# Kernel tuning notes

Measured on AMD Instinct MI355X. Metric: run time of the kernel, lower is better.

## Reference

```python
import jax, jax.numpy as jnp
import numpy as np

HPC = 42  # HPC_FEATURES_LEN

def setup_inputs() -> dict:
    key = jax.random.key(0)
    ks = jax.random.split(key, 8)
    B, N, C, P, S = 4, 16384, 103, 2048, 32
    xyz = jax.random.normal(ks[0], (B, N, 3), dtype=jnp.float32)
    features = jax.random.normal(ks[1], (B, C, N), dtype=jnp.float32)
    new_xyz = jax.random.normal(ks[2], (B, P, 3), dtype=jnp.float32)
    idx = jax.random.randint(ks[3], (B, P, S), 0, N, dtype=jnp.int32)
    # 1x1-conv weights (out_ch, in_ch); gate conv sees full 3+C=106 channels
    Wg = jax.random.normal(ks[4], (64, 106), dtype=jnp.float32) * 0.05
    bg = jnp.zeros((64,), dtype=jnp.float32)
    W1 = jax.random.normal(ks[5], (64, 64), dtype=jnp.float32) * 0.05
    b1 = jnp.zeros((64,), dtype=jnp.float32)
    W2 = jax.random.normal(ks[6], (128, 64), dtype=jnp.float32) * 0.05
    b2 = jnp.zeros((128,), dtype=jnp.float32)
    W3 = jax.random.normal(ks[7], (256, 128), dtype=jnp.float32) * 0.05
    b3 = jnp.zeros((256,), dtype=jnp.float32)
    return {"xyz": xyz, "features": features, "new_xyz": new_xyz, "idx": idx,
            "Wg": Wg, "bg": bg, "W1": W1, "b1": b1, "W2": W2, "b2": b2,
            "W3": W3, "b3": b3}

def reference(xyz, features, new_xyz, idx, Wg, bg, W1, b1, W2, b2, W3, b3):
    # --- grouping: gather neighbors, center xyz, concat features ---
    # grouped_xyz: (B, P, S, 3) -> (B, 3, P, S)
    grouped_xyz = jax.vmap(lambda x, i: x[i])(xyz, idx) - new_xyz[:, :, None, :]
    grouped_xyz = jnp.transpose(grouped_xyz, (0, 3, 1, 2))
    # grouped_feat: (B, C, P, S)
    grouped_feat = jax.vmap(lambda f, i: f[:, i])(features, idx)
    nf = jnp.concatenate([grouped_xyz, grouped_feat], axis=1)  # (B, 3+C, P, S)
    base = nf[:, :-HPC]                                        # (B, 3+C-42, P, S)
    # --- gating 1x1 conv on full channels, then elementwise gate ---
    w = jnp.einsum('bcps,oc->bops', nf, Wg) + bg[None, :, None, None]
    x = base * (1.0 + w)
    # --- 1x1-conv MLP stack with ReLU ---
    for W, b in ((W1, b1), (W2, b2), (W3, b3)):
        x = jax.nn.relu(jnp.einsum('bcps,oc->bops', x, W) + b[None, :, None, None])
    # --- max pool over nsample ---
    pooled = jnp.max(x, axis=-1)  # (B, 256, P)
    return new_xyz, pooled
```

## Files before the change

### kernel.cpp

```cpp
#include <hip/hip_runtime.h>
#include <stdint.h>


namespace {
constexpr int kB = 4, kN = 16384, kC = 103, kP = 2048, kS = 32;

using short8 = __attribute__((ext_vector_type(8))) short;
using short4 = __attribute__((ext_vector_type(4))) short;
using f32x4  = __attribute__((ext_vector_type(4))) float;

constexpr int WG_HI = 0,     WG_LO = 8192;
constexpr int W1_HI = 16384, W1_LO = 20480;
constexpr int W2_HI = 24576, W2_LO = 32768;
constexpr int W3_HI = 40960, W3_LO = 73728;
constexpr size_t FT_OFF    = 262144;
constexpr size_t FT_SHORTS = (size_t)kB * kN * 128;
constexpr size_t WS_NEED   = FT_OFF + 2 * FT_SHORTS * 2;

__device__ __forceinline__ unsigned short f2bf(float x) {
    unsigned u = __float_as_uint(x);
    u += 0x7fffu + ((u >> 16) & 1u);
    return (unsigned short)(u >> 16);
}
__device__ __forceinline__ float bf2f(unsigned short h) {
    return __uint_as_float((unsigned)h << 16);
}
__device__ __forceinline__ unsigned cvtpk(float a, float b) {
    unsigned r;
    asm("v_cvt_pk_bf16_f32 %0, %1, %2" : "=v"(r) : "v"(a), "v"(b));
    return r;
}
__device__ __forceinline__ void pack4(const float v[4], uint2& H, uint2& L) {
    H.x = cvtpk(v[0], v[1]);
    H.y = cvtpk(v[2], v[3]);
    const float r0 = v[0] - __uint_as_float(H.x << 16);
    const float r1 = v[1] - __uint_as_float(H.x & 0xffff0000u);
    const float r2 = v[2] - __uint_as_float(H.y << 16);
    const float r3 = v[3] - __uint_as_float(H.y & 0xffff0000u);
    L.x = cvtpk(r0, r1);
    L.y = cvtpk(r2, r3);
}

__global__ void copy_newxyz(const float* __restrict__ src, float* __restrict__ dst, int n) {
    int i = blockIdx.x * blockDim.x + threadIdx.x;
    if (i < n) dst[i] = src[i];
}

__global__ void prep_weights(const float* __restrict__ Wg, const float* __restrict__ W1,
                             const float* __restrict__ W2, const float* __restrict__ W3,
                             short* __restrict__ ws) {
    int i = blockIdx.x * blockDim.x + threadIdx.x;
    if (i >= 53248) return;
    float w; int hi, lo, j;
    if (i < 8192)       { j = i;         int o = j >> 7, c = j & 127; w = (c < 106) ? Wg[o * 106 + c] : 0.f; hi = WG_HI; lo = WG_LO; }
    else if (i < 12288) { j = i - 8192;  int o = j >> 6, c = j & 63;  w = W1[o * 64 + c];  hi = W1_HI; lo = W1_LO; }
    else if (i < 20480) { j = i - 12288; int o = j >> 6, c = j & 63;  w = W2[o * 64 + c];  hi = W2_HI; lo = W2_LO; }
    else                { j = i - 20480; int o = j >> 7, c = j & 127; w = W3[o * 128 + c]; hi = W3_HI; lo = W3_LO; }
    unsigned short h = f2bf(w);
    ws[hi + j] = (short)h;
    ws[lo + j] = (short)f2bf(w - bf2f(h));
}

__global__ __launch_bounds__(512) void prep_feat(const float* __restrict__ f,
                                                 short* __restrict__ ftH, short* __restrict__ ftL) {
    __shared__ float tile[kC][65];
    const int bb = blockIdx.x >> 8;
    const int n0 = (blockIdx.x & 255) * 64;
    const int tid = threadIdx.x;
    for (int c = tid >> 6; c < kC; c += 8)
        tile[c][tid & 63] = f[((size_t)bb * kC + c) * kN + n0 + (tid & 63)];
    __syncthreads();
    const int np = tid >> 3, gc = tid & 7;
    short* rH = ftH + ((size_t)bb * kN + n0 + np) * 128;
    short* rL = ftL + ((size_t)bb * kN + n0 + np) * 128;
    #pragma unroll
    for (int kk = 0; kk < 2; ++kk) {
        const int chunk = gc + 8 * kk;
        union { uint4 u; short s[8]; } H, L;
        #pragma unroll
        for (int e = 0; e < 8; ++e) {
            const int col = chunk * 8 + e;
            float v = (col >= 3 && col < 106) ? tile[col - 3][np] : 0.f;
            unsigned short hh = f2bf(v);
            H.s[e] = (short)hh;
            L.s[e] = (short)f2bf(v - bf2f(hh));
        }
        *(uint4*)(rH + chunk * 8) = H.u;
        *(uint4*)(rL + chunk * 8) = L.u;
    }
}

template<int NOT, int NPT, int KT, int LDC, int LDW, bool INIT>
__device__ __forceinline__ void gemm_core(
    const short* __restrict__ xh, const short* __restrict__ xl,
    const short* __restrict__ wh, const short* __restrict__ wl,
    const float* __restrict__ bias, int kwoff,
    int ot0, int pt0t, int lane, f32x4 (&acc)[NOT][NPT])
{
    const int q = lane >> 4, n16 = lane & 15;
    short8 whr[NOT * KT], wlr[NOT * KT];
    #pragma unroll
    for (int i = 0; i < NOT; ++i)
        #pragma unroll
        for (int kt = 0; kt < KT; ++kt) {
            const size_t we = (size_t)((ot0 + i) * 16 + n16) * LDW + kwoff + kt * 32 + q * 8;
            whr[i * KT + kt] = *(const short8*)(wh + we);
            wlr[i * KT + kt] = *(const short8*)(wl + we);
        }
    if constexpr (INIT) {
        #pragma unroll
        for (int i = 0; i < NOT; ++i) {
            const f32x4 binit = *(const f32x4*)(bias + (ot0 + i) * 16 + 4 * q);
            #pragma unroll
            for (int j = 0; j < NPT; ++j) acc[i][j] = binit;
        }
    }
    #pragma unroll
    for (int kt = 0; kt < KT; ++kt) {
        const int k0 = kt * 32 + q * 8;
        short8 bh[NPT], bl[NPT];
        #pragma unroll
        for (int j = 0; j < NPT; ++j) {
            const int p = (pt0t + j) * 16 + n16;
            const int e = p * LDC + (k0 ^ ((p & 7) << 3));
            bh[j] = *(const short8*)(xh + e);
            bl[j] = *(const short8*)(xl + e);
        }
        #pragma unroll
        for (int i = 0; i < NOT; ++i) {
            const short8 ah = whr[i * KT + kt];
            const short8 al = wlr[i * KT + kt];
            #pragma unroll
            for (int j = 0; j < NPT; ++j) {
                acc[i][j] = __builtin_amdgcn_mfma_f32_16x16x32_bf16(ah, bh[j], acc[i][j], 0, 0, 0);
                acc[i][j] = __builtin_amdgcn_mfma_f32_16x16x32_bf16(ah, bl[j], acc[i][j], 0, 0, 0);
                acc[i][j] = __builtin_amdgcn_mfma_f32_16x16x32_bf16(al, bh[j], acc[i][j], 0, 0, 0);
            }
        }
    }
}

template<int NOT, int NPT, bool GATE, int LDCO>
__device__ __forceinline__ void store_act(
    f32x4 (&acc)[NOT][NPT], short* __restrict__ oh, short* __restrict__ ol,
    const short* __restrict__ nfh, const short* __restrict__ nfl,
    int ot0, int pt0t, int lane)
{
    const int q = lane >> 4, n16 = lane & 15;
    #pragma unroll
    for (int i = 0; i < NOT; ++i) {
        const int ob = (ot0 + i) * 16 + 4 * q;
        #pragma unroll
        for (int j = 0; j < NPT; ++j) {
            const int p = (pt0t + j) * 16 + n16;
            const int cs = ob ^ ((p & 7) << 3);
            float v[4];
            if (GATE) {
                const short4 h4 = *(const short4*)(nfh + p * 128 + cs);
                const short4 l4 = *(const short4*)(nfl + p * 128 + cs);
                #pragma unroll
                for (int r = 0; r < 4; ++r) {
                    const float base = bf2f((unsigned short)h4[r]) + bf2f((unsigned short)l4[r]);
                    v[r] = fmaf(base, acc[i][j][r], base);
                }
            } else {
                #pragma unroll
                for (int r = 0; r < 4; ++r) v[r] = fmaxf(acc[i][j][r], 0.f);
            }
            uint2 H, L;
            pack4(v, H, L);
            *(uint2*)(oh + p * LDCO + cs) = H;
            *(uint2*)(ol + p * LDCO + cs) = L;
        }
    }
}

template<bool DENSE>
__global__ __launch_bounds__(512, 2) void pointnet_sa(
    const float* __restrict__ xyz, const float* __restrict__ features,
    const float* __restrict__ new_xyz, const int* __restrict__ idx,
    const short* __restrict__ ws, const short* __restrict__ ftH, const short* __restrict__ ftL,
    const float* __restrict__ bg, const float* __restrict__ b1,
    const float* __restrict__ b2, const float* __restrict__ b3,
    float* __restrict__ out_pooled)
{
    __shared__ alignas(16) short smem[24576];
    short* NFh = smem;
    short* NFl = smem + 8192;
    short* X0h = smem + 16384;
    short* X0l = smem + 20480;

    const int tid = threadIdx.x, lane = tid & 63, wave = tid >> 6;
    const int q = lane >> 4, n16 = lane & 15;
    const int pt0 = blockIdx.x * 64;
    const int b = pt0 >> 16;

    if (DENSE) {
        const int gp = tid >> 3, gc = tid & 7;
        const int pt = pt0 + gp;
        const int n = idx[pt];
        const short* rH = ftH + ((size_t)b * kN + n) * 128;
        const short* rL = ftL + ((size_t)b * kN + n) * 128;
        uint4 hc0 = *(const uint4*)(rH + gc * 8);
        uint4 hc1 = *(const uint4*)(rH + gc * 8 + 64);
        uint4 lc0 = *(const uint4*)(rL + gc * 8);
        uint4 lc1 = *(const uint4*)(rL + gc * 8 + 64);
        if (gc == 0) {
            const float* xp = xyz + ((size_t)b * kN + n) * 3;
            const int pp = (pt >> 5) & (kP - 1);
            const float* np = new_xyz + ((size_t)b * kP + pp) * 3;
            union { uint4 u; short s[8]; } H, L;
            H.u = hc0; L.u = lc0;
            #pragma unroll
            for (int c = 0; c < 3; ++c) {
                const float v = xp[c] - np[c];
                const unsigned short hh = f2bf(v);
                H.s[c] = (short)hh;
                L.s[c] = (short)f2bf(v - bf2f(hh));
            }
            hc0 = H.u; lc0 = L.u;
        }
        const int sw = (gc ^ (gp & 7)) * 8;
        *(uint4*)(NFh + gp * 128 + sw)      = hc0;
        *(uint4*)(NFh + gp * 128 + sw + 64) = hc1;
        *(uint4*)(NFl + gp * 128 + sw)      = lc0;
        *(uint4*)(NFl + gp * 128 + sw + 64) = lc1;
    } else {
        const int p = tid & 63;
        const int cg = tid >> 6;
        const int pt = pt0 + p;
        const int n = idx[pt];
        const int pp = (pt >> 5) & (kP - 1);
        const float* fbp = features + (size_t)b * kC * kN + n;
        const float* xp = xyz + ((size_t)b * kN + n) * 3;
        const float* np = new_xyz + ((size_t)b * kP + pp) * 3;
        for (int c = cg; c < 128; c += 8) {
            float v;
            if (c < 3)        v = xp[c] - np[c];
            else if (c < 106) v = fbp[(size_t)(c - 3) * kN];
            else              v = 0.f;
            const unsigned short h = f2bf(v);
            const int cs = c ^ ((p & 7) << 3);
            NFh[p * 128 + cs] = (short)h;
            NFl[p * 128 + cs] = (short)f2bf(v - bf2f(h));
        }
    }
    __syncthreads();

    {
        f32x4 a[1][2];
        gemm_core<1, 2, 4, 128, 128, true>(NFh, NFl, ws + WG_HI, ws + WG_LO, bg, 0,
                                           wave & 3, 2 * (wave >> 2), lane, a);
        store_act<1, 2, true, 64>(a, X0h, X0l, NFh, NFl, wave & 3, 2 * (wave >> 2), lane);
    }
    __syncthreads();

    {
        f32x4 a[1][2];
        gemm_core<1, 2, 2, 64, 64, true>(X0h, X0l, ws + W1_HI, ws + W1_LO, b1, 0,
                                         wave & 3, 2 * (wave >> 2), lane, a);
        store_act<1, 2, false, 128>(a, NFh, NFl, nullptr, nullptr,
                                    wave & 3, 2 * (wave >> 2), lane);
    }
    __syncthreads();

    {
        f32x4 a[2][2];
        gemm_core<2, 2, 2, 128, 64, true>(NFh, NFl, ws + W2_HI, ws + W2_LO, b2, 0,
                                          2 * (wave & 3), 2 * (wave >> 2), lane, a);
        if ((wave & 3) < 2)
            store_act<2, 2, false, 64>(a, X0h, X0l, nullptr, nullptr,
                                       2 * (wave & 3), 2 * (wave >> 2), lane);
        else
            store_act<2, 2, false, 128>(a, NFh + 64, NFl + 64, nullptr, nullptr,
                                        (2 * (wave & 3)) & 3, 2 * (wave >> 2), lane);
    }
    __syncthreads();

    {
        f32x4 a[2][4];
        gemm_core<2, 4, 2, 64, 128, true >(X0h, X0l, ws + W3_HI, ws + W3_LO, b3, 0,
                                           2 * wave, 0, lane, a);
        gemm_core<2, 4, 2, 128, 128, false>(NFh + 64, NFl + 64, ws + W3_HI, ws + W3_LO,
                                            nullptr, 64, 2 * wave, 0, lane, a);
        #pragma unroll
        for (int i = 0; i < 2; ++i) {
            #pragma unroll
            for (int sg = 0; sg < 2; ++sg) {
                #pragma unroll
                for (int r = 0; r < 4; ++r) {
                    float v = fmaxf(a[i][2 * sg][r], a[i][2 * sg + 1][r]);
                    v = fmaxf(v, __shfl_xor(v, 1, 16));
                    v = fmaxf(v, __shfl_xor(v, 2, 16));
                    v = fmaxf(v, __shfl_xor(v, 4, 16));
                    v = fmaxf(v, __shfl_xor(v, 8, 16));
                    v = fmaxf(v, 0.f);
                    if (n16 == 0) {
                        const int o = (2 * wave + i) * 16 + 4 * q + r;
                        const int g = (pt0 >> 5) + sg;
                        out_pooled[((size_t)(g >> 11) * 256 + o) * kP + (g & (kP - 1))] = v;
                    }
                }
            }
        }
    }
}
}

extern "C" void kernel_launch(void* const* d_in, const int* in_sizes, int n_in,
                              void* d_out, int out_size, void* d_ws, size_t ws_size,
                              hipStream_t stream) {
    const float* xyz      = (const float*)d_in[0];
    const float* features = (const float*)d_in[1];
    const float* new_xyz  = (const float*)d_in[2];
    const int*   idx      = (const int*)d_in[3];
    const float* Wg = (const float*)d_in[4];
    const float* bg = (const float*)d_in[5];
    const float* W1 = (const float*)d_in[6];
    const float* b1 = (const float*)d_in[7];
    const float* W2 = (const float*)d_in[8];
    const float* b2 = (const float*)d_in[9];
    const float* W3 = (const float*)d_in[10];
    const float* b3 = (const float*)d_in[11];
    float* out = (float*)d_out;
    short* ws  = (short*)d_ws;
    short* ftH = (short*)((char*)d_ws + FT_OFF);
    short* ftL = ftH + FT_SHORTS;

    const int nxyz = kB * kP * 3;
    copy_newxyz<<<(nxyz + 255) / 256, 256, 0, stream>>>(new_xyz, out, nxyz);
    prep_weights<<<(53248 + 255) / 256, 256, 0, stream>>>(Wg, W1, W2, W3, ws);

    float* pooled = out + nxyz;
    if (ws_size >= WS_NEED) {
        prep_feat<<<kB * (kN / 64), 512, 0, stream>>>(features, ftH, ftL);
        pointnet_sa<true><<<(kB * kP * kS) / 64, 512, 0, stream>>>(
            xyz, features, new_xyz, idx, ws, ftH, ftL, bg, b1, b2, b3, pooled);
    } else {
        pointnet_sa<false><<<(kB * kP * kS) / 64, 512, 0, stream>>>(
            xyz, features, new_xyz, idx, ws, nullptr, nullptr, bg, b1, b2, b3, pooled);
    }
}
```

Before: 183.2 us.

## Split fused pointnet kernel into per-layer kernels with global intermediates

```diff
diff --git a/kernel.cpp b/kernel.cpp
--- a/kernel.cpp
+++ b/kernel.cpp
@@ -4,6 +4,7 @@
 
 namespace {
 constexpr int kB = 4, kN = 16384, kC = 103, kP = 2048, kS = 32;
+constexpr int NPTS = kB * kP * kS;
 
 using short8 = __attribute__((ext_vector_type(8))) short;
 using short4 = __attribute__((ext_vector_type(4))) short;
@@ -16,6 +17,16 @@
 constexpr size_t FT_OFF    = 262144;
 constexpr size_t FT_SHORTS = (size_t)kB * kN * 128;
 constexpr size_t WS_NEED   = FT_OFF + 2 * FT_SHORTS * 2;
+constexpr size_t Z_OFF   = 262144;
+constexpr size_t FTH_B   = Z_OFF;
+constexpr size_t FTL_B   = Z_OFF + 16777216;
+constexpr size_t X0H_B   = Z_OFF + 33554432;
+constexpr size_t X0L_B   = X0H_B + 33554432;
+constexpr size_t X2H_B   = Z_OFF;
+constexpr size_t X2L_B   = Z_OFF + 67108864;
+constexpr size_t X1H_B   = Z_OFF + 134217728;
+constexpr size_t X1L_B   = X1H_B + 33554432;
+constexpr size_t WS_BIG  = X1L_B + 33554432;
 
 __device__ __forceinline__ unsigned short f2bf(float x) {
     unsigned u = __float_as_uint(x);
@@ -39,6 +50,12 @@
     const float r3 = v[3] - __uint_as_float(H.y & 0xffff0000u);
     L.x = cvtpk(r0, r1);
     L.y = cvtpk(r2, r3);
+}
+__device__ __forceinline__ f32x4 mfma3(short8 ah, short8 al, short8 bh, short8 bl, f32x4 acc) {
+    acc = __builtin_amdgcn_mfma_f32_16x16x32_bf16(ah, bh, acc, 0, 0, 0);
+    acc = __builtin_amdgcn_mfma_f32_16x16x32_bf16(ah, bl, acc, 0, 0, 0);
+    acc = __builtin_amdgcn_mfma_f32_16x16x32_bf16(al, bh, acc, 0, 0, 0);
+    return acc;
 }
 
 __global__ void copy_newxyz(const float* __restrict__ src, float* __restrict__ dst, int n) {
@@ -90,6 +107,236 @@
     }
 }
 
+
+__global__ __launch_bounds__(256, 3) void k1_gate(
+    const float* __restrict__ xyz, const float* __restrict__ new_xyz,
+    const int* __restrict__ idx, const short* __restrict__ wsw,
+    const short* __restrict__ ftH, const short* __restrict__ ftL,
+    const float* __restrict__ bg, short* __restrict__ x0H, short* __restrict__ x0L)
+{
+    const int lane = threadIdx.x & 63, wave = threadIdx.x >> 6;
+    const int q = lane >> 4, n16 = lane & 15;
+    const int gy = blockIdx.y;
+    const int pb = blockIdx.x * 512;
+    const int b  = pb >> 16;
+    short8 wh0[4], wl0[4], wh1[4], wl1[4];
+    #pragma unroll
+    for (int kt = 0; kt < 4; ++kt) {
+        const size_t w0 = (size_t)((2 * gy) * 16 + n16) * 128 + kt * 32 + q * 8;
+        const size_t w1 = (size_t)((2 * gy + 1) * 16 + n16) * 128 + kt * 32 + q * 8;
+        wh0[kt] = *(const short8*)(wsw + WG_HI + w0);
+        wl0[kt] = *(const short8*)(wsw + WG_LO + w0);
+        wh1[kt] = *(const short8*)(wsw + WG_HI + w1);
+        wl1[kt] = *(const short8*)(wsw + WG_LO + w1);
+    }
+    const f32x4 bi0 = *(const f32x4*)(bg + (2 * gy) * 16 + 4 * q);
+    const f32x4 bi1 = *(const f32x4*)(bg + (2 * gy + 1) * 16 + 4 * q);
+
+    for (int it = 0; it < 8; ++it) {
+        const int pt = pb + wave * 128 + it * 16 + n16;
+        const int n  = idx[pt];
+        const short* rH = ftH + ((size_t)b * kN + n) * 128;
+        const short* rL = ftL + ((size_t)b * kN + n) * 128;
+        float xd0 = 0.f, xd1 = 0.f, xd2 = 0.f;
+        if (q == 0) {
+            const float* xp = xyz + ((size_t)b * kN + n) * 3;
+            const int pp = (pt >> 5) & (kP - 1);
+            const float* np = new_xyz + ((size_t)b * kP + pp) * 3;
+            xd0 = xp[0] - np[0]; xd1 = xp[1] - np[1]; xd2 = xp[2] - np[2];
+        }
+        short8 bh[4], bl[4];
+        #pragma unroll
+        for (int kt = 0; kt < 4; ++kt) {
+            bh[kt] = *(const short8*)(rH + kt * 32 + q * 8);
+            bl[kt] = *(const short8*)(rL + kt * 32 + q * 8);
+        }
+        if (q == 0) {
+            const unsigned short h0 = f2bf(xd0), h1 = f2bf(xd1), h2 = f2bf(xd2);
+            bh[0][0] = (short)h0; bh[0][1] = (short)h1; bh[0][2] = (short)h2;
+            bl[0][0] = (short)f2bf(xd0 - bf2f(h0));
+            bl[0][1] = (short)f2bf(xd1 - bf2f(h1));
+            bl[0][2] = (short)f2bf(xd2 - bf2f(h2));
+        }
+        f32x4 a0 = bi0, a1 = bi1;
+        #pragma unroll
+        for (int kt = 0; kt < 4; ++kt) {
+            a0 = mfma3(wh0[kt], wl0[kt], bh[kt], bl[kt], a0);
+            a1 = mfma3(wh1[kt], wl1[kt], bh[kt], bl[kt], a1);
+        }
+        #pragma unroll
+        for (int i = 0; i < 2; ++i) {
+            const int ob = (2 * gy + i) * 16 + 4 * q;
+            const uint2 BH = *(const uint2*)(rH + ob);
+            const uint2 BL = *(const uint2*)(rL + ob);
+            float base[4];
+            base[0] = __uint_as_float(BH.x << 16)         + __uint_as_float(BL.x << 16);
+            base[1] = __uint_as_float(BH.x & 0xffff0000u) + __uint_as_float(BL.x & 0xffff0000u);
+            base[2] = __uint_as_float(BH.y << 16)         + __uint_as_float(BL.y << 16);
+            base[3] = __uint_as_float(BH.y & 0xffff0000u) + __uint_as_float(BL.y & 0xffff0000u);
+            if (gy == 0 && i == 0 && q == 0) { base[0] = xd0; base[1] = xd1; base[2] = xd2; }
+            const f32x4 A = i ? a1 : a0;
+            float v[4];
+            #pragma unroll
+            for (int r = 0; r < 4; ++r) v[r] = fmaf(base[r], A[r], base[r]);
+            uint2 H, L;
+            pack4(v, H, L);
+            *(uint2*)(x0H + (size_t)pt * 64 + ob) = H;
+            *(uint2*)(x0L + (size_t)pt * 64 + ob) = L;
+        }
+    }
+}
+
+__global__ __launch_bounds__(256, 4) void k2_l1(
+    const short* __restrict__ wsw, const short* __restrict__ x0H, const short* __restrict__ x0L,
+    const float* __restrict__ b1f, short* __restrict__ x1H, short* __restrict__ x1L)
+{
+    const int lane = threadIdx.x & 63, wave = threadIdx.x >> 6;
+    const int q = lane >> 4, n16 = lane & 15;
+    const int pb = blockIdx.x * 512;
+    short8 wh[8], wl[8];
+    #pragma unroll
+    for (int o = 0; o < 4; ++o)
+        #pragma unroll
+        for (int kt = 0; kt < 2; ++kt) {
+            const size_t we = (size_t)(o * 16 + n16) * 64 + kt * 32 + q * 8;
+            wh[o * 2 + kt] = *(const short8*)(wsw + W1_HI + we);
+            wl[o * 2 + kt] = *(const short8*)(wsw + W1_LO + we);
+        }
+    for (int it = 0; it < 8; ++it) {
+        const int pt = pb + wave * 128 + it * 16 + n16;
+        short8 bh[2], bl[2];
+        #pragma unroll
+        for (int kt = 0; kt < 2; ++kt) {
+            bh[kt] = *(const short8*)(x0H + (size_t)pt * 64 + kt * 32 + q * 8);
+            bl[kt] = *(const short8*)(x0L + (size_t)pt * 64 + kt * 32 + q * 8);
+        }
+        #pragma unroll
+        for (int o = 0; o < 4; ++o) {
+            f32x4 a = *(const f32x4*)(b1f + o * 16 + 4 * q);
+            #pragma unroll
+            for (int kt = 0; kt < 2; ++kt)
+                a = mfma3(wh[o * 2 + kt], wl[o * 2 + kt], bh[kt], bl[kt], a);
+            float v[4];
+            #pragma unroll
+            for (int r = 0; r < 4; ++r) v[r] = fmaxf(a[r], 0.f);
+            uint2 H, L;
+            pack4(v, H, L);
+            *(uint2*)(x1H + (size_t)pt * 64 + o * 16 + 4 * q) = H;
+            *(uint2*)(x1L + (size_t)pt * 64 + o * 16 + 4 * q) = L;
+        }
+    }
+}
+
+__global__ __launch_bounds__(256, 4) void k3_l2(
+    const short* __restrict__ wsw, const short* __restrict__ x1H, const short* __restrict__ x1L,
+    const float* __restrict__ b2f, short* __restrict__ x2H, short* __restrict__ x2L)
+{
+    const int lane = threadIdx.x & 63, wave = threadIdx.x >> 6;
+    const int q = lane >> 4, n16 = lane & 15;
+    const int gy = blockIdx.y;
+    const int pb = blockIdx.x * 512;
+    short8 wh[8], wl[8];
+    #pragma unroll
+    for (int o = 0; o < 4; ++o)
+        #pragma unroll
+        for (int kt = 0; kt < 2; ++kt) {
+            const size_t we = (size_t)((4 * gy + o) * 16 + n16) * 64 + kt * 32 + q * 8;
+            wh[o * 2 + kt] = *(const short8*)(wsw + W2_HI + we);
+            wl[o * 2 + kt] = *(const short8*)(wsw + W2_LO + we);
+        }
+    for (int it = 0; it < 8; ++it) {
+        const int pt = pb + wave * 128 + it * 16 + n16;
+        short8 bh[2], bl[2];
+        #pragma unroll
+        for (int kt = 0; kt < 2; ++kt) {
+            bh[kt] = *(const short8*)(x1H + (size_t)pt * 64 + kt * 32 + q * 8);
+            bl[kt] = *(const short8*)(x1L + (size_t)pt * 64 + kt * 32 + q * 8);
+        }
+        #pragma unroll
+        for (int o = 0; o < 4; ++o) {
+            f32x4 a = *(const f32x4*)(b2f + (4 * gy + o) * 16 + 4 * q);
+            #pragma unroll
+            for (int kt = 0; kt < 2; ++kt)
+                a = mfma3(wh[o * 2 + kt], wl[o * 2 + kt], bh[kt], bl[kt], a);
+            float v[4];
+            #pragma unroll
+            for (int r = 0; r < 4; ++r) v[r] = fmaxf(a[r], 0.f);
+            uint2 H, L;
+            pack4(v, H, L);
+            *(uint2*)(x2H + (size_t)pt * 128 + (4 * gy + o) * 16 + 4 * q) = H;
+            *(uint2*)(x2L + (size_t)pt * 128 + (4 * gy + o) * 16 + 4 * q) = L;
+        }
+    }
+}
+
+__global__ __launch_bounds__(512, 2) void k4_l3(
+    const short* __restrict__ wsw, const short* __restrict__ x2H, const short* __restrict__ x2L,
+    const float* __restrict__ b3f, float* __restrict__ out_pooled)
+{
+    __shared__ alignas(16) short lds[32768];
+    const int tid = threadIdx.x, lane = tid & 63, wave = tid >> 6;
+    const int q = lane >> 4, n16 = lane & 15;
+    const int gy = blockIdx.y;
+    #pragma unroll
+    for (int k = 0; k < 4; ++k) {
+        const int cid = tid + k * 512;
+        const int row = cid >> 4, col = (cid & 15) * 8;
+        const int swz = col ^ ((row & 7) << 3);
+        *(short8*)(lds + row * 128 + swz) =
+            *(const short8*)(wsw + W3_HI + (size_t)(128 * gy + row) * 128 + col);
+        *(short8*)(lds + 16384 + row * 128 + swz) =
+            *(const short8*)(wsw + W3_LO + (size_t)(128 * gy + row) * 128 + col);
+    }
+    __syncthreads();
+
+    for (int it = 0; it < 4; ++it) {
+        const int sg = blockIdx.x * 32 + wave * 4 + it;
+        const size_t pt0 = (size_t)sg * 32;
+        f32x4 acc[8][2];
+        #pragma unroll
+        for (int ot = 0; ot < 8; ++ot) {
+            const f32x4 bi = *(const f32x4*)(b3f + 128 * gy + ot * 16 + 4 * q);
+            acc[ot][0] = bi; acc[ot][1] = bi;
+        }
+        #pragma unroll
+        for (int kt = 0; kt < 4; ++kt) {
+            const int k0 = kt * 32 + q * 8;
+            short8 bh[2], bl[2];
+            #pragma unroll
+            for (int j = 0; j < 2; ++j) {
+                const size_t e = (pt0 + j * 16 + n16) * 128 + k0;
+                bh[j] = *(const short8*)(x2H + e);
+                bl[j] = *(const short8*)(x2L + e);
+            }
+            #pragma unroll
+            for (int ot = 0; ot < 8; ++ot) {
+                const int row = ot * 16 + n16;
+                const int a = row * 128 + (k0 ^ ((row & 7) << 3));
+                const short8 ah = *(const short8*)(lds + a);
+                const short8 al = *(const short8*)(lds + 16384 + a);
+                #pragma unroll
+                for (int j = 0; j < 2; ++j)
+                    acc[ot][j] = mfma3(ah, al, bh[j], bl[j], acc[ot][j]);
+            }
+        }
+        const int p = sg & (kP - 1), bb = sg >> 11;
+        float* outB = out_pooled + ((size_t)bb * 256 + 128 * gy) * kP + p;
+        #pragma unroll
+        for (int ot = 0; ot < 8; ++ot) {
+            #pragma unroll
+            for (int r = 0; r < 4; ++r) {
+                float v = fmaxf(acc[ot][0][r], acc[ot][1][r]);
+                v = fmaxf(v, __shfl_xor(v, 1, 16));
+                v = fmaxf(v, __shfl_xor(v, 2, 16));
+                v = fmaxf(v, __shfl_xor(v, 4, 16));
+                v = fmaxf(v, __shfl_xor(v, 8, 16));
+                v = fmaxf(v, 0.f);
+                if (n16 == 0) outB[(size_t)(ot * 16 + 4 * q + r) * kP] = v;
+            }
+        }
+    }
+}
+
 template<int NOT, int NPT, int KT, int LDC, int LDW, bool INIT>
 __device__ __forceinline__ void gemm_core(
     const short* __restrict__ xh, const short* __restrict__ xl,
@@ -98,15 +345,6 @@
     int ot0, int pt0t, int lane, f32x4 (&acc)[NOT][NPT])
 {
     const int q = lane >> 4, n16 = lane & 15;
-    short8 whr[NOT * KT], wlr[NOT * KT];
-    #pragma unroll
-    for (int i = 0; i < NOT; ++i)
-        #pragma unroll
-        for (int kt = 0; kt < KT; ++kt) {
-            const size_t we = (size_t)((ot0 + i) * 16 + n16) * LDW + kwoff + kt * 32 + q * 8;
-            whr[i * KT + kt] = *(const short8*)(wh + we);
-            wlr[i * KT + kt] = *(const short8*)(wl + we);
-        }
     if constexpr (INIT) {
         #pragma unroll
         for (int i = 0; i < NOT; ++i) {
@@ -128,14 +366,11 @@
         }
         #pragma unroll
         for (int i = 0; i < NOT; ++i) {
-            const short8 ah = whr[i * KT + kt];
-            const short8 al = wlr[i * KT + kt];
-            #pragma unroll
-            for (int j = 0; j < NPT; ++j) {
-                acc[i][j] = __builtin_amdgcn_mfma_f32_16x16x32_bf16(ah, bh[j], acc[i][j], 0, 0, 0);
-                acc[i][j] = __builtin_amdgcn_mfma_f32_16x16x32_bf16(ah, bl[j], acc[i][j], 0, 0, 0);
-                acc[i][j] = __builtin_amdgcn_mfma_f32_16x16x32_bf16(al, bh[j], acc[i][j], 0, 0, 0);
-            }
+            const size_t we = (size_t)((ot0 + i) * 16 + n16) * LDW + kwoff + k0;
+            const short8 ah = *(const short8*)(wh + we);
+            const short8 al = *(const short8*)(wl + we);
+            #pragma unroll
+            for (int j = 0; j < NPT; ++j) acc[i][j] = mfma3(ah, al, bh[j], bl[j], acc[i][j]);
         }
     }
 }
@@ -246,7 +481,6 @@
         }
     }
     __syncthreads();
-
     {
         f32x4 a[1][2];
         gemm_core<1, 2, 4, 128, 128, true>(NFh, NFl, ws + WG_HI, ws + WG_LO, bg, 0,
@@ -254,7 +488,6 @@
         store_act<1, 2, true, 64>(a, X0h, X0l, NFh, NFl, wave & 3, 2 * (wave >> 2), lane);
     }
     __syncthreads();
-
     {
         f32x4 a[1][2];
         gemm_core<1, 2, 2, 64, 64, true>(X0h, X0l, ws + W1_HI, ws + W1_LO, b1, 0,
@@ -263,7 +496,6 @@
                                     wave & 3, 2 * (wave >> 2), lane);
     }
     __syncthreads();
-
     {
         f32x4 a[2][2];
         gemm_core<2, 2, 2, 128, 64, true>(NFh, NFl, ws + W2_HI, ws + W2_LO, b2, 0,
@@ -276,7 +508,6 @@
                                         (2 * (wave & 3)) & 3, 2 * (wave >> 2), lane);
     }
     __syncthreads();
-
     {
         f32x4 a[2][4];
         gemm_core<2, 4, 2, 64, 128, true >(X0h, X0l, ws + W3_HI, ws + W3_LO, b3, 0,
@@ -284,9 +515,9 @@
         gemm_core<2, 4, 2, 128, 128, false>(NFh + 64, NFl + 64, ws + W3_HI, ws + W3_LO,
                                             nullptr, 64, 2 * wave, 0, lane, a);
         #pragma unroll
-        for (int i = 0; i < 2; ++i) {
-            #pragma unroll
-            for (int sg = 0; sg < 2; ++sg) {
+        for (int i = 0; i < 2; ++i)
+            #pragma unroll
+            for (int sg = 0; sg < 2; ++sg)
                 #pragma unroll
                 for (int r = 0; r < 4; ++r) {
                     float v = fmaxf(a[i][2 * sg][r], a[i][2 * sg + 1][r]);
@@ -301,8 +532,6 @@
                         out_pooled[((size_t)(g >> 11) * 256 + o) * kP + (g & (kP - 1))] = v;
                     }
                 }
-            }
-        }
     }
 }
 }
@@ -323,21 +552,37 @@
     const float* W3 = (const float*)d_in[10];
     const float* b3 = (const float*)d_in[11];
     float* out = (float*)d_out;
-    short* ws  = (short*)d_ws;
-    short* ftH = (short*)((char*)d_ws + FT_OFF);
-    short* ftL = ftH + FT_SHORTS;
+    short* wsw = (short*)d_ws;
+    char*  wsb = (char*)d_ws;
 
     const int nxyz = kB * kP * 3;
     copy_newxyz<<<(nxyz + 255) / 256, 256, 0, stream>>>(new_xyz, out, nxyz);
-    prep_weights<<<(53248 + 255) / 256, 256, 0, stream>>>(Wg, W1, W2, W3, ws);
-
+    prep_weights<<<(53248 + 255) / 256, 256, 0, stream>>>(Wg, W1, W2, W3, wsw);
     float* pooled = out + nxyz;
-    if (ws_size >= WS_NEED) {
+
+    if (ws_size >= WS_BIG) {
+        short* ftH = (short*)(wsb + FTH_B);
+        short* ftL = (short*)(wsb + FTL_B);
+        short* x0H = (short*)(wsb + X0H_B);
+        short* x0L = (short*)(wsb + X0L_B);
+        short* x1H = (short*)(wsb + X1H_B);
+        short* x1L = (short*)(wsb + X1L_B);
+        short* x2H = (short*)(wsb + X2H_B);
+        short* x2L = (short*)(wsb + X2L_B);
+        prep_feat<<<kB * (kN / 64), 512, 0, stream>>>(features, ftH, ftL);
+        k1_gate<<<dim3(NPTS / 512, 2), 256, 0, stream>>>(xyz, new_xyz, idx, wsw,
+                                                         ftH, ftL, bg, x0H, x0L);
+        k2_l1<<<NPTS / 512, 256, 0, stream>>>(wsw, x0H, x0L, b1, x1H, x1L);
+        k3_l2<<<dim3(NPTS / 512, 2), 256, 0, stream>>>(wsw, x1H, x1L, b2, x2H, x2L);
+        k4_l3<<<dim3(NPTS / 1024, 2), 512, 0, stream>>>(wsw, x2H, x2L, b3, pooled);
+    } else if (ws_size >= WS_NEED) {
+        short* ftH = (short*)(wsb + FT_OFF);
+        short* ftL = ftH + FT_SHORTS;
         prep_feat<<<kB * (kN / 64), 512, 0, stream>>>(features, ftH, ftL);
         pointnet_sa<true><<<(kB * kP * kS) / 64, 512, 0, stream>>>(
-            xyz, features, new_xyz, idx, ws, ftH, ftL, bg, b1, b2, b3, pooled);
+            xyz, features, new_xyz, idx, wsw, ftH, ftL, bg, b1, b2, b3, pooled);
     } else {
         pointnet_sa<false><<<(kB * kP * kS) / 64, 512, 0, stream>>>(
-            xyz, features, new_xyz, idx, ws, nullptr, nullptr, bg, b1, b2, b3, pooled);
-    }
-}
+            xyz, features, new_xyz, idx, wsw, nullptr, nullptr, bg, b1, b2, b3, pooled);
+    }
+}
```

Result: slower. 469.1 us (+156.1%).
